# Kernel optimization log

Hardware: AMD Instinct MI355X
Metric: run time of the kernel (lower is better)

Reference implementation:

```python
import jax, jax.numpy as jnp
import numpy as np

N, E = 50000, 1600000            # nodes, edges
IN, H, OUT = 128, 128, 64        # in_channels, hidden_channels, out_channels
EPS = 1e-5                       # BatchNorm eps


def setup_inputs() -> dict:
    key = jax.random.key(0)
    ks = jax.random.split(key, 9)
    glorot = lambda k, shp, fan: jax.random.normal(k, shp, jnp.float32) * (1.0 / np.sqrt(fan))
    return {
        "x": jax.random.normal(ks[0], (N, IN), jnp.float32),
        "edge_index": jax.random.randint(ks[1], (2, E), 0, N),
        # layer 0: SAGEConv(IN, H) + BatchNorm(H)
        "Wl0": glorot(ks[2], (H, IN), IN), "Wr0": glorot(ks[3], (H, IN), IN),
        "b0": jnp.zeros((H,), jnp.float32),
        "g0": jnp.ones((H,), jnp.float32), "be0": jnp.zeros((H,), jnp.float32),
        # layer 1: SAGEConv(H, H) + BatchNorm(H)
        "Wl1": glorot(ks[4], (H, H), H), "Wr1": glorot(ks[5], (H, H), H),
        "b1": jnp.zeros((H,), jnp.float32),
        "g1": jnp.ones((H,), jnp.float32), "be1": jnp.zeros((H,), jnp.float32),
        # layer 2: SAGEConv(H, OUT)
        "Wl2": glorot(ks[6], (OUT, H), H), "Wr2": glorot(ks[7], (OUT, H), H),
        "b2": jnp.zeros((OUT,), jnp.float32),
    }


def _sage_conv(x, src, dst, Wl, Wr, b):
    """PyG SAGEConv with mean aggregation: lin_l(mean_{j->i} x_j) + lin_r(x_i) + b."""
    deg = jax.ops.segment_sum(jnp.ones((src.shape[0],), x.dtype), dst, num_segments=N)
    agg = jax.ops.segment_sum(x[src], dst, num_segments=N)  # [N, d] scatter-sum of gathered msgs
    agg = agg / jnp.maximum(deg, 1.0)[:, None]              # scatter-mean (0 for isolated nodes)
    return agg @ Wl.T + x @ Wr.T + b


def _batchnorm(x, gamma, beta):
    # training-mode BN over the node dimension (batch statistics)
    mu = jnp.mean(x, axis=0)
    var = jnp.var(x, axis=0)
    return (x - mu) * jax.lax.rsqrt(var + EPS) * gamma + beta


def reference(x, edge_index, Wl0, Wr0, b0, g0, be0, Wl1, Wr1, b1, g1, be1, Wl2, Wr2, b2):
    src, dst = edge_index[0], edge_index[1]
    h = jax.nn.relu(_batchnorm(_sage_conv(x, src, dst, Wl0, Wr0, b0), g0, be0))
    h = jax.nn.relu(_batchnorm(_sage_conv(h, src, dst, Wl1, Wr1, b1), g1, be1))
    return _sage_conv(h, src, dst, Wl2, Wr2, b2)
```

## Files before the change

kernel.cpp:

```cpp
#include <hip/hip_runtime.h>

#define NND 50000
#define NED 1600000
#define EPSBN 1e-5f
#define NB 196
#define EPB 8192
#define SCELEM (NB * NB)

typedef __attribute__((ext_vector_type(8))) short short8;
typedef __attribute__((ext_vector_type(4))) float f32x4;

__device__ __forceinline__ float bf_lo(unsigned u) {
    union { unsigned u; float f; } c; c.u = u << 16; return c.f;
}
__device__ __forceinline__ float bf_hi(unsigned u) {
    union { unsigned u; float f; } c; c.u = u & 0xffff0000u; return c.f;
}
__device__ __forceinline__ unsigned short f2b(float f) {
    union { float f; unsigned u; } c; c.f = f;
    unsigned r = (c.u + 0x7fffu + ((c.u >> 16) & 1u)) >> 16;
    return (unsigned short)r;
}

__global__ __launch_bounds__(256) void cast_bf16_kernel(const float* __restrict__ x,
                                                        unsigned short* __restrict__ xb) {
    int i = blockIdx.x * 256 + threadIdx.x;
    if (i >= NND * 16) return;
    const float4* p = (const float4*)x + (size_t)i * 2;
    float4 a = p[0], b = p[1];
    uint4 o;
    o.x = f2b(a.x) | ((unsigned)f2b(a.y) << 16);
    o.y = f2b(a.z) | ((unsigned)f2b(a.w) << 16);
    o.z = f2b(b.x) | ((unsigned)f2b(b.y) << 16);
    o.w = f2b(b.z) | ((unsigned)f2b(b.w) << 16);
    ((uint4*)xb)[i] = o;
}

__global__ __launch_bounds__(256) void eb_hist_kernel(const int* __restrict__ dst,
                                                      int* __restrict__ cnt) {
    __shared__ int hs[256];
    int t = threadIdx.x;
    hs[t] = 0;
    __syncthreads();
    int base = blockIdx.x * EPB;
    for (int i = t; i < EPB; i += 256) {
        int e = base + i;
        if (e < NED) atomicAdd(&hs[dst[e] >> 8], 1);
    }
    __syncthreads();
    if (t < NB) cnt[blockIdx.x * NB + t] = hs[t];
}

__global__ __launch_bounds__(1024) void eb_scan_kernel(int* __restrict__ cnt,
                                                       int* __restrict__ binOff,
                                                       int* __restrict__ rowptr) {
    __shared__ int s[1024];
    const int t = threadIdx.x;
    const int CH = (SCELEM + 1023) / 1024;
    const int i0 = t * CH;
    int sum = 0;
    for (int i = 0; i < CH; ++i) {
        int idx = i0 + i;
        if (idx < SCELEM) {
            int bin = idx / NB, blk = idx - bin * NB;
            sum += cnt[blk * NB + bin];
        }
    }
    s[t] = sum;
    __syncthreads();
    for (int o = 1; o < 1024; o <<= 1) {
        int a = (t >= o) ? s[t - o] : 0;
        __syncthreads();
        s[t] += a;
        __syncthreads();
    }
    int pre = s[t] - sum;
    for (int i = 0; i < CH; ++i) {
        int idx = i0 + i;
        if (idx < SCELEM) {
            int bin = idx / NB, blk = idx - bin * NB;
            int* p = &cnt[blk * NB + bin];
            int v = *p; *p = pre; pre += v;
        }
    }
    __syncthreads();
    for (int b = t; b < NB; b += 1024) binOff[b] = cnt[b];
    if (t == 0) { binOff[NB] = NED; rowptr[NND] = NED; }
}

__global__ __launch_bounds__(256) void eb_scatter_kernel(const int* __restrict__ src,
                                                         const int* __restrict__ dst,
                                                         const int* __restrict__ off,
                                                         unsigned* __restrict__ pairs) {
    __shared__ int cur[256];
    int t = threadIdx.x;
    if (t < NB) cur[t] = off[blockIdx.x * NB + t];
    __syncthreads();
    int base = blockIdx.x * EPB;
    for (int i = t; i < EPB; i += 256) {
        int e = base + i;
        if (e < NED) {
            int d = dst[e];
            int pos = atomicAdd(&cur[d >> 8], 1);
            pairs[pos] = ((unsigned)src[e] << 8) | (unsigned)(d & 255);
        }
    }
}

__global__ __launch_bounds__(256) void bucket_finalize_kernel(const unsigned* __restrict__ pairs,
                                                              const int* __restrict__ binOff,
                                                              int* __restrict__ rowptr,
                                                              float* __restrict__ dinv,
                                                              int* __restrict__ csr) {
    __shared__ int hist[256], s[256], cur[256];
    int b = blockIdx.x, t = threadIdx.x;
    int beg = binOff[b], end = binOff[b + 1];
    hist[t] = 0;
    __syncthreads();
    for (int e = beg + t; e < end; e += 256)
        atomicAdd(&hist[pairs[e] & 255u], 1);
    __syncthreads();
    int v = hist[t];
    s[t] = v;
    __syncthreads();
#pragma unroll
    for (int o = 1; o < 256; o <<= 1) {
        int a = (t >= o) ? s[t - o] : 0;
        __syncthreads();
        s[t] += a;
        __syncthreads();
    }
    int base = beg + s[t] - v;
    int node = b * 256 + t;
    if (node < NND) {
        rowptr[node] = base;
        dinv[node] = 1.0f / (float)(v > 1 ? v : 1);
    }
    cur[t] = base;
    __syncthreads();
    for (int e = beg + t; e < end; e += 256) {
        unsigned p = pairs[e];
        int pos = atomicAdd(&cur[p & 255u], 1);
        csr[pos] = (int)(p >> 8);
    }
}

__global__ __launch_bounds__(256) void gather128_kernel(const unsigned short* __restrict__ xb,
                                                        const int* __restrict__ rowptr,
                                                        const int* __restrict__ csr,
                                                        const float* __restrict__ dinv,
                                                        unsigned short* __restrict__ aggb) {
    int w = threadIdx.x >> 6;
    int node = blockIdx.x * 4 + w;
    if (node >= NND) return;
    int lane = threadIdx.x & 63;
    int q = lane >> 4;
    int c8 = lane & 15;
    int beg = rowptr[node], end = rowptr[node + 1];
    const uint4* xv = (const uint4*)xb;

    float acc[8];
#pragma unroll
    for (int i = 0; i < 8; ++i) acc[i] = 0.f;

    for (int j = beg + q; j < end; j += 4) {
        int s = csr[j];
        uint4 v = xv[(size_t)s * 16 + c8];
        acc[0] += bf_lo(v.x); acc[1] += bf_hi(v.x);
        acc[2] += bf_lo(v.y); acc[3] += bf_hi(v.y);
        acc[4] += bf_lo(v.z); acc[5] += bf_hi(v.z);
        acc[6] += bf_lo(v.w); acc[7] += bf_hi(v.w);
    }
#pragma unroll
    for (int i = 0; i < 8; ++i) {
        acc[i] += __shfl_xor(acc[i], 16);
        acc[i] += __shfl_xor(acc[i], 32);
    }
    if (q == 0) {
        float dv = dinv[node];
        uint4 o;
        o.x = f2b(acc[0] * dv) | ((unsigned)f2b(acc[1] * dv) << 16);
        o.y = f2b(acc[2] * dv) | ((unsigned)f2b(acc[3] * dv) << 16);
        o.z = f2b(acc[4] * dv) | ((unsigned)f2b(acc[5] * dv) << 16);
        o.w = f2b(acc[6] * dv) | ((unsigned)f2b(acc[7] * dv) << 16);
        ((uint4*)aggb)[(size_t)node * 16 + c8] = o;
    }
}

__global__ __launch_bounds__(256) void gather64_kernel(const unsigned short* __restrict__ tb,
                                                       const int* __restrict__ rowptr,
                                                       const int* __restrict__ csr,
                                                       const float* __restrict__ dinv,
                                                       float* __restrict__ out) {
    int w = threadIdx.x >> 6;
    int node = blockIdx.x * 4 + w;
    if (node >= NND) return;
    int lane = threadIdx.x & 63;
    int g = lane >> 3;
    int c8 = lane & 7;
    int beg = rowptr[node], end = rowptr[node + 1];
    const uint4* tv = (const uint4*)tb;

    float acc[8];
#pragma unroll
    for (int i = 0; i < 8; ++i) acc[i] = 0.f;

    for (int j = beg + g; j < end; j += 8) {
        int s = csr[j];
        uint4 v = tv[(size_t)s * 8 + c8];
        acc[0] += bf_lo(v.x); acc[1] += bf_hi(v.x);
        acc[2] += bf_lo(v.y); acc[3] += bf_hi(v.y);
        acc[4] += bf_lo(v.z); acc[5] += bf_hi(v.z);
        acc[6] += bf_lo(v.w); acc[7] += bf_hi(v.w);
    }
#pragma unroll
    for (int i = 0; i < 8; ++i) {
        acc[i] += __shfl_xor(acc[i], 8);
        acc[i] += __shfl_xor(acc[i], 16);
        acc[i] += __shfl_xor(acc[i], 32);
    }
    if (g == 0) {
        float dv = dinv[node];
        float* po = out + (size_t)node * 64 + c8 * 8;
        float4 a = *(float4*)po, b = *(float4*)(po + 4);
        a.x += acc[0] * dv; a.y += acc[1] * dv; a.z += acc[2] * dv; a.w += acc[3] * dv;
        b.x += acc[4] * dv; b.y += acc[5] * dv; b.z += acc[6] * dv; b.w += acc[7] * dv;
        *(float4*)po = a; *(float4*)(po + 4) = b;
    }
}

__global__ __launch_bounds__(256) void pack_all_kernel(const float* __restrict__ Wl0,
                                                       const float* __restrict__ Wr0,
                                                       const float* __restrict__ Wl1,
                                                       const float* __restrict__ Wr1,
                                                       const float* __restrict__ Wl2,
                                                       const float* __restrict__ Wr2,
                                                       unsigned short* __restrict__ wp0,
                                                       unsigned short* __restrict__ wp1,
                                                       unsigned short* __restrict__ wp2,
                                                       float* __restrict__ stats) {
    int blk = blockIdx.x;
    if (blk == 0) { stats[threadIdx.x] = 0.f; stats[256 + threadIdx.x] = 0.f; }
    const float *Wl, *Wr; unsigned short* wp; bool l2f; int t;
    if (blk < 16)      { Wl = Wl0; Wr = Wr0; wp = wp0; l2f = false; t = blk * 256 + threadIdx.x; }
    else if (blk < 32) { Wl = Wl1; Wr = Wr1; wp = wp1; l2f = false; t = (blk - 16) * 256 + threadIdx.x; }
    else               { Wl = Wl2; Wr = Wr2; wp = wp2; l2f = true;  t = (blk - 32) * 256 + threadIdx.x; }
    int rem = t & 511;
    int ks = t >> 9;
    int cf = rem >> 6, l = rem & 63;
    int c = cf * 16 + (l & 15);
    int kb = ks * 32 + ((l >> 4) * 8);
    unsigned short v[8];
#pragma unroll
    for (int j = 0; j < 8; ++j) {
        int k = kb + j;
        float w;
        if (l2f) w = (c < 64) ? Wl[c * 128 + k] : Wr[(c - 64) * 128 + k];
        else     w = (k < 128) ? Wl[c * 128 + k] : Wr[c * 128 + (k - 128)];
        v[j] = f2b(w);
    }
    uint4 o;
    o.x = v[0] | ((unsigned)v[1] << 16);
    o.y = v[2] | ((unsigned)v[3] << 16);
    o.z = v[4] | ((unsigned)v[5] << 16);
    o.w = v[6] | ((unsigned)v[7] << 16);
    ((uint4*)wp)[t] = o;
}

template<int KS, int MODE>
__global__ __launch_bounds__(256) void gemm_mfma_kernel(const unsigned short* __restrict__ aggb,
                                                        const unsigned short* xinb,
                                                        const unsigned short* __restrict__ wpack,
                                                        const float* __restrict__ bias,
                                                        void* outv,
                                                        unsigned short* __restrict__ tbuf,
                                                        float* __restrict__ stats) {
    constexpr int NCF = 8, NCOL = 128;
    constexpr bool ST = (MODE == 0);
    __shared__ float o_s[64][NCOL + 4];
    __shared__ float sum_s[ST ? 4 : 1][ST ? 128 : 1];
    __shared__ float sq_s[ST ? 4 : 1][ST ? 128 : 1];

    const int t = threadIdx.x, wave = t >> 6, lane = t & 63;
    const int row0 = blockIdx.x * 64;
    const int arow = row0 + wave * 16 + (lane & 15);
    const bool avalid = arow < NND;
    const int ko = (lane >> 4) * 8;

    f32x4 acc[NCF];
#pragma unroll
    for (int cf = 0; cf < NCF; ++cf) acc[cf] = (f32x4){0.f, 0.f, 0.f, 0.f};

    const short8* wp = (const short8*)wpack;
#pragma unroll
    for (int ks = 0; ks < KS; ++ks) {
        short8 a = {0, 0, 0, 0, 0, 0, 0, 0};
        if (avalid) {
            int k = ks * 32 + ko;
            const unsigned short* base;
            if (MODE == 0)
                base = (k < 128) ? (aggb + (size_t)arow * 128 + k)
                                 : (xinb + (size_t)arow * 128 + (k - 128));
            else
                base = xinb + (size_t)arow * 128 + k;
            a = *(const short8*)base;
        }
#pragma unroll
        for (int cf = 0; cf < NCF; ++cf) {
            short8 b = wp[(ks * NCF + cf) * 64 + lane];
            acc[cf] = __builtin_amdgcn_mfma_f32_16x16x32_bf16(a, b, acc[cf], 0, 0, 0);
        }
    }

#pragma unroll
    for (int cf = 0; cf < NCF; ++cf)
#pragma unroll
        for (int r = 0; r < 4; ++r)
            o_s[wave * 16 + (lane >> 4) * 4 + r][cf * 16 + (lane & 15)] = acc[cf][r];

    if (ST) {
#pragma unroll
        for (int cf = 0; cf < NCF; ++cf) {
            float s = acc[cf][0] + acc[cf][1] + acc[cf][2] + acc[cf][3];
            float q = acc[cf][0] * acc[cf][0] + acc[cf][1] * acc[cf][1]
                    + acc[cf][2] * acc[cf][2] + acc[cf][3] * acc[cf][3];
            s += __shfl_xor(s, 16); s += __shfl_xor(s, 32);
            q += __shfl_xor(q, 16); q += __shfl_xor(q, 32);
            if (lane < 16) {
                sum_s[wave][cf * 16 + lane] = s;
                sq_s[wave][cf * 16 + lane] = q;
            }
        }
    }
    __syncthreads();

    const int r = t >> 2, q = t & 3;
    const int grow = row0 + r;
    if (grow < NND) {
        if (MODE == 0) {
            unsigned short* out = (unsigned short*)outv;
            const int c0 = q * 32;
#pragma unroll
            for (int g = 0; g < 4; ++g) {
                float v0 = o_s[r][c0 + g * 8 + 0], v1 = o_s[r][c0 + g * 8 + 1];
                float v2 = o_s[r][c0 + g * 8 + 2], v3 = o_s[r][c0 + g * 8 + 3];
                float v4 = o_s[r][c0 + g * 8 + 4], v5 = o_s[r][c0 + g * 8 + 5];
                float v6 = o_s[r][c0 + g * 8 + 6], v7 = o_s[r][c0 + g * 8 + 7];
                uint4 o;
                o.x = f2b(v0) | ((unsigned)f2b(v1) << 16);
                o.y = f2b(v2) | ((unsigned)f2b(v3) << 16);
                o.z = f2b(v4) | ((unsigned)f2b(v5) << 16);
                o.w = f2b(v6) | ((unsigned)f2b(v7) << 16);
                ((uint4*)(out + (size_t)grow * NCOL + c0))[g] = o;
            }
        } else {
            if (q < 2) {
                const int c0 = q * 32;
#pragma unroll
                for (int g = 0; g < 4; ++g) {
                    float v0 = o_s[r][c0 + g * 8 + 0], v1 = o_s[r][c0 + g * 8 + 1];
                    float v2 = o_s[r][c0 + g * 8 + 2], v3 = o_s[r][c0 + g * 8 + 3];
                    float v4 = o_s[r][c0 + g * 8 + 4], v5 = o_s[r][c0 + g * 8 + 5];
                    float v6 = o_s[r][c0 + g * 8 + 6], v7 = o_s[r][c0 + g * 8 + 7];
                    uint4 o;
                    o.x = f2b(v0) | ((unsigned)f2b(v1) << 16);
                    o.y = f2b(v2) | ((unsigned)f2b(v3) << 16);
                    o.z = f2b(v4) | ((unsigned)f2b(v5) << 16);
                    o.w = f2b(v6) | ((unsigned)f2b(v7) << 16);
                    ((uint4*)(tbuf + (size_t)grow * 64 + c0))[g] = o;
                }
            } else {
                float* out = (float*)outv;
                const int c0 = (q - 2) * 32;
#pragma unroll
                for (int g = 0; g < 8; ++g) {
                    float4 o;
                    o.x = o_s[r][64 + c0 + g * 4 + 0] + bias[c0 + g * 4 + 0];
                    o.y = o_s[r][64 + c0 + g * 4 + 1] + bias[c0 + g * 4 + 1];
                    o.z = o_s[r][64 + c0 + g * 4 + 2] + bias[c0 + g * 4 + 2];
                    o.w = o_s[r][64 + c0 + g * 4 + 3] + bias[c0 + g * 4 + 3];
                    ((float4*)(out + (size_t)grow * 64 + c0))[g] = o;
                }
            }
        }
    }

    if (ST && t < 128) {
        float s = sum_s[0][t] + sum_s[1][t] + sum_s[2][t] + sum_s[3][t];
        float q2 = sq_s[0][t] + sq_s[1][t] + sq_s[2][t] + sq_s[3][t];
        unsafeAtomicAdd(&stats[t], s);
        unsafeAtomicAdd(&stats[128 + t], q2);
    }
}

__global__ __launch_bounds__(256) void bn_relu_kernel(unsigned short* __restrict__ h,
                                                      const float* __restrict__ stats,
                                                      const float* __restrict__ gamma,
                                                      const float* __restrict__ beta) {
    __shared__ float ab_s[256];
    int t = threadIdx.x;
    if (t < 128) {
        float mu = stats[t] * (1.0f / NND);
        float var = stats[128 + t] * (1.0f / NND) - mu * mu;
        float rs = rsqrtf(var + EPSBN);
        float a = gamma[t] * rs;
        ab_s[t] = a;
        ab_s[128 + t] = beta[t] - mu * a;
    }
    __syncthreads();
    int i = blockIdx.x * 256 + t;
    if (i >= NND * 16) return;
    uint4 v = ((uint4*)h)[i];
    int c0 = (i & 15) * 8;
    float o[8] = {bf_lo(v.x), bf_hi(v.x), bf_lo(v.y), bf_hi(v.y),
                  bf_lo(v.z), bf_hi(v.z), bf_lo(v.w), bf_hi(v.w)};
#pragma unroll
    for (int j = 0; j < 8; ++j)
        o[j] = fmaxf(o[j] * ab_s[c0 + j] + ab_s[128 + c0 + j], 0.f);
    uint4 w;
    w.x = f2b(o[0]) | ((unsigned)f2b(o[1]) << 16);
    w.y = f2b(o[2]) | ((unsigned)f2b(o[3]) << 16);
    w.z = f2b(o[4]) | ((unsigned)f2b(o[5]) << 16);
    w.w = f2b(o[6]) | ((unsigned)f2b(o[7]) << 16);
    ((uint4*)h)[i] = w;
}

extern "C" void kernel_launch(void* const* d_in, const int* in_sizes, int n_in,
                              void* d_out, int out_size, void* d_ws, size_t ws_size,
                              hipStream_t stream) {
    const float* x   = (const float*)d_in[0];
    const int*   ei  = (const int*)d_in[1];
    const int* src = ei;
    const int* dst = ei + NED;
    const float* Wl0 = (const float*)d_in[2];
    const float* Wr0 = (const float*)d_in[3];
    const float* g0  = (const float*)d_in[5];
    const float* be0 = (const float*)d_in[6];
    const float* Wl1 = (const float*)d_in[7];
    const float* Wr1 = (const float*)d_in[8];
    const float* g1  = (const float*)d_in[10];
    const float* be1 = (const float*)d_in[11];
    const float* Wl2 = (const float*)d_in[12];
    const float* Wr2 = (const float*)d_in[13];
    const float* b2  = (const float*)d_in[14];
    float* out = (float*)d_out;

    const size_t NF = (size_t)NND * 128;
    unsigned short* aggb = (unsigned short*)d_ws;
    unsigned short* xb   = aggb + NF;
    unsigned short* h    = xb + NF;
    int*   csr    = (int*)(h + NF);
    float* dinv   = (float*)(csr + NED);
    int*   rowptr = (int*)(dinv + NND);
    int*   binOff = rowptr + NND + 8;
    int*   cnt    = binOff + 256;
    unsigned short* wp0 = (unsigned short*)(cnt + 38420);
    unsigned short* wp1 = wp0 + 32768;
    unsigned short* wp2 = wp1 + 32768;
    float* stats  = (float*)(wp2 + 32768);
    unsigned* pairs = (unsigned*)aggb;

    const int GB = (NND + 3) / 4;
    const int GM = (NND + 63) / 64;

    cast_bf16_kernel<<<(NND * 16 + 255) / 256, 256, 0, stream>>>(x, xb);
    eb_hist_kernel<<<NB, 256, 0, stream>>>(dst, cnt);
    eb_scan_kernel<<<1, 1024, 0, stream>>>(cnt, binOff, rowptr);
    eb_scatter_kernel<<<NB, 256, 0, stream>>>(src, dst, cnt, pairs);
    bucket_finalize_kernel<<<NB, 256, 0, stream>>>(pairs, binOff, rowptr, dinv, csr);
    pack_all_kernel<<<40, 256, 0, stream>>>(Wl0, Wr0, Wl1, Wr1, Wl2, Wr2, wp0, wp1, wp2, stats);

    gather128_kernel<<<GB, 256, 0, stream>>>(xb, rowptr, csr, dinv, aggb);
    gemm_mfma_kernel<8, 0><<<GM, 256, 0, stream>>>(aggb, xb, wp0, nullptr, h, nullptr, stats);
    bn_relu_kernel<<<(NND * 16 + 255) / 256, 256, 0, stream>>>(h, stats, g0, be0);

    gather128_kernel<<<GB, 256, 0, stream>>>(h, rowptr, csr, dinv, aggb);
    gemm_mfma_kernel<8, 0><<<GM, 256, 0, stream>>>(aggb, h, wp1, nullptr, h, nullptr, stats + 256);
    bn_relu_kernel<<<(NND * 16 + 255) / 256, 256, 0, stream>>>(h, stats + 256, g1, be1);

    gemm_mfma_kernel<4, 2><<<GM, 256, 0, stream>>>(nullptr, h, wp2, b2, out, xb, nullptr);
    gather64_kernel<<<GB, 256, 0, stream>>>(xb, rowptr, csr, dinv, out);
}
```

Baseline: 484.2 us.

## Parallelize bucket offset scan and split gathers across feature-column groups

The single-block serial scan over the bin×block count matrix is replaced by a three-kernel parallel scan over a transposed, padded count layout, which the histogram kernel now writes directly. The gather kernels are re-split so each block handles one column slice (64 bytes) of a node's features, with 16 edges processed concurrently per wavefront instead of 4 or 8. The scan change targets a latency-bound single-block kernel. The gather change aims for more memory-level parallelism on low-degree rows. It costs more launches, extra shuffle reductions, and re-reading each row's CSR indices once per column group.

```diff
diff --git a/kernel.cpp b/kernel.cpp
--- a/kernel.cpp
+++ b/kernel.cpp
@@ -6,6 +6,7 @@
 #define NB 196
 #define EPB 8192
 #define SCELEM (NB * NB)
+#define SCPAD (38 * 1024)
 
 typedef __attribute__((ext_vector_type(8))) short short8;
 typedef __attribute__((ext_vector_type(4))) float f32x4;
@@ -37,10 +38,13 @@
 }
 
 __global__ __launch_bounds__(256) void eb_hist_kernel(const int* __restrict__ dst,
-                                                      int* __restrict__ cnt) {
+                                                      int* __restrict__ cntT) {
     __shared__ int hs[256];
     int t = threadIdx.x;
     hs[t] = 0;
+    if (blockIdx.x == 0) {
+        for (int i = t; i < SCPAD - SCELEM; i += 256) cntT[SCELEM + i] = 0;
+    }
     __syncthreads();
     int base = blockIdx.x * EPB;
     for (int i = t; i < EPB; i += 256) {
@@ -48,25 +52,16 @@
         if (e < NED) atomicAdd(&hs[dst[e] >> 8], 1);
     }
     __syncthreads();
-    if (t < NB) cnt[blockIdx.x * NB + t] = hs[t];
-}
-
-__global__ __launch_bounds__(1024) void eb_scan_kernel(int* __restrict__ cnt,
-                                                       int* __restrict__ binOff,
-                                                       int* __restrict__ rowptr) {
+    if (t < NB) cntT[t * NB + blockIdx.x] = hs[t];
+}
+
+__global__ __launch_bounds__(1024) void scan_p1_kernel(int* __restrict__ cnt,
+                                                       int* __restrict__ psum) {
     __shared__ int s[1024];
-    const int t = threadIdx.x;
-    const int CH = (SCELEM + 1023) / 1024;
-    const int i0 = t * CH;
-    int sum = 0;
-    for (int i = 0; i < CH; ++i) {
-        int idx = i0 + i;
-        if (idx < SCELEM) {
-            int bin = idx / NB, blk = idx - bin * NB;
-            sum += cnt[blk * NB + bin];
-        }
-    }
-    s[t] = sum;
+    int t = threadIdx.x;
+    int idx = blockIdx.x * 1024 + t;
+    int v = cnt[idx];
+    s[t] = v;
     __syncthreads();
     for (int o = 1; o < 1024; o <<= 1) {
         int a = (t >= o) ? s[t - o] : 0;
@@ -74,27 +69,45 @@
         s[t] += a;
         __syncthreads();
     }
-    int pre = s[t] - sum;
-    for (int i = 0; i < CH; ++i) {
-        int idx = i0 + i;
-        if (idx < SCELEM) {
-            int bin = idx / NB, blk = idx - bin * NB;
-            int* p = &cnt[blk * NB + bin];
-            int v = *p; *p = pre; pre += v;
-        }
-    }
-    __syncthreads();
-    for (int b = t; b < NB; b += 1024) binOff[b] = cnt[b];
+    cnt[idx] = s[t] - v;
+    if (t == 1023) psum[blockIdx.x] = s[t];
+}
+
+__global__ __launch_bounds__(64) void scan_p2_kernel(int* __restrict__ psum,
+                                                     int* __restrict__ binOff,
+                                                     int* __restrict__ rowptr) {
+    __shared__ int s[64];
+    int t = threadIdx.x;
+    int v = (t < 38) ? psum[t] : 0;
+    s[t] = v;
+    __syncthreads();
+    for (int o = 1; o < 64; o <<= 1) {
+        int a = (t >= o) ? s[t - o] : 0;
+        __syncthreads();
+        s[t] += a;
+        __syncthreads();
+    }
+    if (t < 38) psum[t] = s[t] - v;
     if (t == 0) { binOff[NB] = NED; rowptr[NND] = NED; }
+}
+
+__global__ __launch_bounds__(1024) void scan_p3_kernel(int* __restrict__ cnt,
+                                                       const int* __restrict__ psum,
+                                                       int* __restrict__ binOff) {
+    int idx = blockIdx.x * 1024 + threadIdx.x;
+    int val = cnt[idx] + psum[blockIdx.x];
+    cnt[idx] = val;
+    int bin = idx / NB;
+    if (bin < NB && idx - bin * NB == 0) binOff[bin] = val;
 }
 
 __global__ __launch_bounds__(256) void eb_scatter_kernel(const int* __restrict__ src,
                                                          const int* __restrict__ dst,
-                                                         const int* __restrict__ off,
+                                                         const int* __restrict__ offT,
                                                          unsigned* __restrict__ pairs) {
     __shared__ int cur[256];
     int t = threadIdx.x;
-    if (t < NB) cur[t] = off[blockIdx.x * NB + t];
+    if (t < NB) cur[t] = offT[t * NB + blockIdx.x];
     __syncthreads();
     int base = blockIdx.x * EPB;
     for (int i = t; i < EPB; i += 256) {
@@ -150,12 +163,12 @@
                                                         const int* __restrict__ csr,
                                                         const float* __restrict__ dinv,
                                                         unsigned short* __restrict__ aggb) {
-    int w = threadIdx.x >> 6;
-    int node = blockIdx.x * 4 + w;
+    int g = blockIdx.x & 3;
+    int node = (blockIdx.x >> 2) * 4 + (threadIdx.x >> 6);
     if (node >= NND) return;
     int lane = threadIdx.x & 63;
-    int q = lane >> 4;
-    int c8 = lane & 15;
+    int slot = lane >> 2;
+    int c4 = lane & 3;
     int beg = rowptr[node], end = rowptr[node + 1];
     const uint4* xv = (const uint4*)xb;
 
@@ -163,9 +176,9 @@
 #pragma unroll
     for (int i = 0; i < 8; ++i) acc[i] = 0.f;
 
-    for (int j = beg + q; j < end; j += 4) {
+    for (int j = beg + slot; j < end; j += 16) {
         int s = csr[j];
-        uint4 v = xv[(size_t)s * 16 + c8];
+        uint4 v = xv[(size_t)s * 16 + g * 4 + c4];
         acc[0] += bf_lo(v.x); acc[1] += bf_hi(v.x);
         acc[2] += bf_lo(v.y); acc[3] += bf_hi(v.y);
         acc[4] += bf_lo(v.z); acc[5] += bf_hi(v.z);
@@ -173,17 +186,19 @@
     }
 #pragma unroll
     for (int i = 0; i < 8; ++i) {
+        acc[i] += __shfl_xor(acc[i], 4);
+        acc[i] += __shfl_xor(acc[i], 8);
         acc[i] += __shfl_xor(acc[i], 16);
         acc[i] += __shfl_xor(acc[i], 32);
     }
-    if (q == 0) {
+    if (slot == 0) {
         float dv = dinv[node];
         uint4 o;
         o.x = f2b(acc[0] * dv) | ((unsigned)f2b(acc[1] * dv) << 16);
         o.y = f2b(acc[2] * dv) | ((unsigned)f2b(acc[3] * dv) << 16);
         o.z = f2b(acc[4] * dv) | ((unsigned)f2b(acc[5] * dv) << 16);
         o.w = f2b(acc[6] * dv) | ((unsigned)f2b(acc[7] * dv) << 16);
-        ((uint4*)aggb)[(size_t)node * 16 + c8] = o;
+        ((uint4*)aggb)[(size_t)node * 16 + g * 4 + c4] = o;
     }
 }
 
@@ -192,12 +207,12 @@
                                                        const int* __restrict__ csr,
                                                        const float* __restrict__ dinv,
                                                        float* __restrict__ out) {
-    int w = threadIdx.x >> 6;
-    int node = blockIdx.x * 4 + w;
+    int g = blockIdx.x & 1;
+    int node = (blockIdx.x >> 1) * 4 + (threadIdx.x >> 6);
     if (node >= NND) return;
     int lane = threadIdx.x & 63;
-    int g = lane >> 3;
-    int c8 = lane & 7;
+    int slot = lane >> 2;
+    int c4 = lane & 3;
     int beg = rowptr[node], end = rowptr[node + 1];
     const uint4* tv = (const uint4*)tb;
 
@@ -205,9 +220,9 @@
 #pragma unroll
     for (int i = 0; i < 8; ++i) acc[i] = 0.f;
 
-    for (int j = beg + g; j < end; j += 8) {
+    for (int j = beg + slot; j < end; j += 16) {
         int s = csr[j];
-        uint4 v = tv[(size_t)s * 8 + c8];
+        uint4 v = tv[(size_t)s * 8 + g * 4 + c4];
         acc[0] += bf_lo(v.x); acc[1] += bf_hi(v.x);
         acc[2] += bf_lo(v.y); acc[3] += bf_hi(v.y);
         acc[4] += bf_lo(v.z); acc[5] += bf_hi(v.z);
@@ -215,13 +230,14 @@
     }
 #pragma unroll
     for (int i = 0; i < 8; ++i) {
+        acc[i] += __shfl_xor(acc[i], 4);
         acc[i] += __shfl_xor(acc[i], 8);
         acc[i] += __shfl_xor(acc[i], 16);
         acc[i] += __shfl_xor(acc[i], 32);
     }
-    if (g == 0) {
+    if (slot == 0) {
         float dv = dinv[node];
-        float* po = out + (size_t)node * 64 + c8 * 8;
+        float* po = out + (size_t)node * 64 + g * 32 + c4 * 8;
         float4 a = *(float4*)po, b = *(float4*)(po + 4);
         a.x += acc[0] * dv; a.y += acc[1] * dv; a.z += acc[2] * dv; a.w += acc[3] * dv;
         b.x += acc[4] * dv; b.y += acc[5] * dv; b.z += acc[6] * dv; b.w += acc[7] * dv;
@@ -453,31 +469,35 @@
     float* dinv   = (float*)(csr + NED);
     int*   rowptr = (int*)(dinv + NND);
     int*   binOff = rowptr + NND + 8;
-    int*   cnt    = binOff + 256;
-    unsigned short* wp0 = (unsigned short*)(cnt + 38420);
+    int*   cntT   = binOff + 256;
+    int*   psum   = cntT + SCPAD;
+    unsigned short* wp0 = (unsigned short*)(psum + 64);
     unsigned short* wp1 = wp0 + 32768;
     unsigned short* wp2 = wp1 + 32768;
     float* stats  = (float*)(wp2 + 32768);
     unsigned* pairs = (unsigned*)aggb;
 
-    const int GB = (NND + 3) / 4;
+    const int G128B = 12500 * 4;
+    const int G64B  = 12500 * 2;
     const int GM = (NND + 63) / 64;
 
     cast_bf16_kernel<<<(NND * 16 + 255) / 256, 256, 0, stream>>>(x, xb);
-    eb_hist_kernel<<<NB, 256, 0, stream>>>(dst, cnt);
-    eb_scan_kernel<<<1, 1024, 0, stream>>>(cnt, binOff, rowptr);
-    eb_scatter_kernel<<<NB, 256, 0, stream>>>(src, dst, cnt, pairs);
+    eb_hist_kernel<<<NB, 256, 0, stream>>>(dst, cntT);
+    scan_p1_kernel<<<38, 1024, 0, stream>>>(cntT, psum);
+    scan_p2_kernel<<<1, 64, 0, stream>>>(psum, binOff, rowptr);
+    scan_p3_kernel<<<38, 1024, 0, stream>>>(cntT, psum, binOff);
+    eb_scatter_kernel<<<NB, 256, 0, stream>>>(src, dst, cntT, pairs);
     bucket_finalize_kernel<<<NB, 256, 0, stream>>>(pairs, binOff, rowptr, dinv, csr);
     pack_all_kernel<<<40, 256, 0, stream>>>(Wl0, Wr0, Wl1, Wr1, Wl2, Wr2, wp0, wp1, wp2, stats);
 
-    gather128_kernel<<<GB, 256, 0, stream>>>(xb, rowptr, csr, dinv, aggb);
+    gather128_kernel<<<G128B, 256, 0, stream>>>(xb, rowptr, csr, dinv, aggb);
     gemm_mfma_kernel<8, 0><<<GM, 256, 0, stream>>>(aggb, xb, wp0, nullptr, h, nullptr, stats);
     bn_relu_kernel<<<(NND * 16 + 255) / 256, 256, 0, stream>>>(h, stats, g0, be0);
 
-    gather128_kernel<<<GB, 256, 0, stream>>>(h, rowptr, csr, dinv, aggb);
+    gather128_kernel<<<G128B, 256, 0, stream>>>(h, rowptr, csr, dinv, aggb);
     gemm_mfma_kernel<8, 0><<<GM, 256, 0, stream>>>(aggb, h, wp1, nullptr, h, nullptr, stats + 256);
     bn_relu_kernel<<<(NND * 16 + 255) / 256, 256, 0, stream>>>(h, stats + 256, g1, be1);
 
     gemm_mfma_kernel<4, 2><<<GM, 256, 0, stream>>>(nullptr, h, wp2, b2, out, xb, nullptr);
-    gather64_kernel<<<GB, 256, 0, stream>>>(xb, rowptr, csr, dinv, out);
-}
+    gather64_kernel<<<G64B, 256, 0, stream>>>(xb, rowptr, csr, dinv, out);
+}
```

New measurement: 512.0 us. 1.06x slower.
